# Performance work log

Hardware: AMD Instinct MI355X
Metric: run time of the kernel (lower is better)

Reference implementation:

```python
import jax, jax.numpy as jnp
import numpy as np

T, B, OBS, A, P, NB, H = 32, 256, 1024, 16, 600, 601, 128


def setup_inputs() -> dict:
    key = jax.random.key(0)
    ks = jax.random.split(key, 32)
    f32 = jnp.float32

    def rn(k, shape, scale):
        return jax.random.normal(k, shape, dtype=f32) * scale

    hh = 1.0 / np.sqrt(H)
    inp = {
        "obs_seq": rn(ks[0], (T, B, OBS), 1.0),
        # backbone MLP (512, 512)
        "bb_w1": rn(ks[1], (OBS, 512), 1.0 / np.sqrt(OBS)), "bb_b1": jnp.zeros((512,), f32),
        "bb_w2": rn(ks[2], (512, 512), 1.0 / np.sqrt(512)), "bb_b2": jnp.zeros((512,), f32),
        # feedforward heads (final layers init std=0.01, bias 0 per module)
        "pol_w": rn(ks[3], (512, A), 0.01), "pol_b": jnp.zeros((A,), f32),
        "y_w": rn(ks[4], (512, P), 0.01), "y_b": jnp.zeros((P,), f32),
        "ci_w": rn(ks[5], (512, H), 1.0 / np.sqrt(512)), "ci_b": jnp.zeros((H,), f32),
        # LSTMCell(A, 128): gate order i,f,g,o as in torch
        "w_ih": rn(ks[6], (A, 4 * H), hh), "w_hh": rn(ks[7], (H, 4 * H), hh),
        "b_ih": rn(ks[8], (4 * H,), hh), "b_hh": rn(ks[9], (4 * H,), hh),
        # z / q / aux_pi MLPs: Linear(128,128) -> ReLU -> Linear(128, out)
        "z_w1": rn(ks[10], (H, H), hh), "z_b1": jnp.zeros((H,), f32),
        "z_w2": rn(ks[11], (H, P), 0.01), "z_b2": jnp.zeros((P,), f32),
        "q_w1": rn(ks[12], (H, H), hh), "q_b1": jnp.zeros((H,), f32),
        "q_w2": rn(ks[13], (H, NB), 0.01), "q_b2": jnp.zeros((NB,), f32),
        "a_w1": rn(ks[14], (H, H), hh), "a_b1": jnp.zeros((H,), f32),
        "a_w2": rn(ks[15], (H, A), 0.01), "a_b2": jnp.zeros((A,), f32),
    }
    return inp


def reference(obs_seq, bb_w1, bb_b1, bb_w2, bb_b2, pol_w, pol_b, y_w, y_b,
              ci_w, ci_b, w_ih, w_hh, b_ih, b_hh,
              z_w1, z_b1, z_w2, z_b2, q_w1, q_b1, q_w2, q_b2,
              a_w1, a_b1, a_w2, a_b2):
    Tn, Bn = obs_seq.shape[:2]
    x = obs_seq.reshape(Tn * Bn, -1)  # feedforward across time: fold T into batch
    emb = jax.nn.relu(jax.nn.relu(x @ bb_w1 + bb_b1) @ bb_w2 + bb_b2)  # [N,512]
    logits = emb @ pol_w + pol_b  # [N,A]
    y = emb @ y_w + y_b           # [N,P]
    c0 = emb @ ci_w + ci_b        # [N,H]
    h0 = jnp.tanh(c0)

    # one_hot(a) @ W_ih^T == row a of W_ih (input-to-gate contribution per action)
    in_gates = w_ih + b_ih  # [A, 4H]

    def step(carry, ig):
        h, c = carry
        g = ig + h @ w_hh + b_hh  # [N,4H]
        i, f, gg, o = jnp.split(g, 4, axis=-1)  # torch gate order i,f,g,o
        c = jax.nn.sigmoid(f) * c + jax.nn.sigmoid(i) * jnp.tanh(gg)
        h = jax.nn.sigmoid(o) * jnp.tanh(c)
        return (h, c), h

    _, h_all = jax.lax.scan(step, (h0, c0), in_gates)  # [A, N, H]

    def mlp(hx, w1, b1, w2, b2):
        return jax.nn.relu(hx @ w1 + b1) @ w2 + b2

    def to_tba(arr):
        Aa, N, D = arr.shape
        return arr.reshape(Aa, Tn, Bn, D).transpose(1, 2, 0, 3)  # [T,B,A,D]

    z = to_tba(mlp(h_all, z_w1, z_b1, z_w2, z_b2))
    q = to_tba(mlp(h_all, q_w1, q_b1, q_w2, q_b2))
    aux_pi = to_tba(mlp(h_all, a_w1, a_b1, a_w2, a_b2))
    return (logits.reshape(Tn, Bn, -1), y.reshape(Tn, Bn, -1), z, q, aux_pi)
```

## Files before the change

kernel.cpp:

```cpp
#include <hip/hip_runtime.h>
#include <stdint.h>

typedef short bf16x8 __attribute__((ext_vector_type(8)));
typedef float f32x4 __attribute__((ext_vector_type(4)));
typedef unsigned short u16x4 __attribute__((ext_vector_type(4)));

__device__ __forceinline__ unsigned short f2b(float f) {
  union { float f; unsigned u; } v; v.f = f;
  unsigned r = v.u + 0x7fffu + ((v.u >> 16) & 1u);
  return (unsigned short)(r >> 16);
}
__device__ __forceinline__ float fsigm(float x) { return 1.f / (1.f + __expf(-x)); }
__device__ __forceinline__ float ftanh(float x) {
  float t = __expf(-2.f * fabsf(x));
  float r = (1.f - t) / (1.f + t);
  return copysignf(r, x);
}

struct TD { const float* in; unsigned short* out; int R, C; };
struct TDs { TD d[12]; };

__global__ __launch_bounds__(256) void tconv_all(TDs ds) {
  TD t = ds.d[blockIdx.z];
  int c0 = blockIdx.x * 32, r0 = blockIdx.y * 32;
  if (c0 >= t.C || r0 >= t.R) return;
  __shared__ float tl[32][33];
  int tx = threadIdx.x & 31, ty = threadIdx.x >> 5;
  #pragma unroll
  for (int i = 0; i < 32; i += 8) {
    int r = r0 + ty + i, c = c0 + tx;
    tl[ty + i][tx] = (r < t.R && c < t.C) ? t.in[(size_t)r * t.C + c] : 0.f;
  }
  __syncthreads();
  #pragma unroll
  for (int i = 0; i < 32; i += 8) {
    int c = c0 + ty + i, r = r0 + tx;
    if (c < t.C && r < t.R) t.out[(size_t)c * t.R + r] = f2b(tl[tx][ty + i]);
  }
}

__global__ __launch_bounds__(256) void conv_k(const float* __restrict__ in,
                                              unsigned short* __restrict__ out, int n) {
  int i = (blockIdx.x * 256 + threadIdx.x) * 8;
  if (i >= n) return;
  float4 a = *(const float4*)(in + i);
  float4 b = *(const float4*)(in + i + 4);
  bf16x8 v;
  v[0] = (short)f2b(a.x); v[1] = (short)f2b(a.y); v[2] = (short)f2b(a.z); v[3] = (short)f2b(a.w);
  v[4] = (short)f2b(b.x); v[5] = (short)f2b(b.y); v[6] = (short)f2b(b.z); v[7] = (short)f2b(b.w);
  *(bf16x8*)(out + i) = v;
}

template <int ACT, bool OBF16>
__global__ __launch_bounds__(256) void gemm_k(const unsigned short* __restrict__ A,
                                              const unsigned short* __restrict__ BT,
                                              const float* __restrict__ bias,
                                              void* __restrict__ Cp,
                                              int M, int N, int K, int ldC) {
  __shared__ unsigned short As[64][40];
  __shared__ unsigned short Bs[64][40];
  const int tid = threadIdx.x;
  const int n0 = blockIdx.x * 64;
  const int m0 = blockIdx.y * 64;
  const int wid = tid >> 6, lane = tid & 63;
  const int wm = (wid >> 1) * 32, wn = (wid & 1) * 32;
  const int lr = lane & 15, lk = lane >> 4;
  const int sr = tid >> 2, sc = (tid & 3) * 8;

  f32x4 acc[2][2] = {};

  for (int k0 = 0; k0 < K; k0 += 32) {
    *(bf16x8*)&As[sr][sc] = *(const bf16x8*)(A + (size_t)(m0 + sr) * K + k0 + sc);
    {
      int n = n0 + sr;
      bf16x8 v = {};
      if (n < N) v = *(const bf16x8*)(BT + (size_t)n * K + k0 + sc);
      *(bf16x8*)&Bs[sr][sc] = v;
    }
    __syncthreads();
    bf16x8 af[2], bfr[2];
    #pragma unroll
    for (int mi = 0; mi < 2; mi++) af[mi] = *(const bf16x8*)&As[wm + mi * 16 + lr][lk * 8];
    #pragma unroll
    for (int ni = 0; ni < 2; ni++) bfr[ni] = *(const bf16x8*)&Bs[wn + ni * 16 + lr][lk * 8];
    #pragma unroll
    for (int mi = 0; mi < 2; mi++)
      #pragma unroll
      for (int ni = 0; ni < 2; ni++)
        acc[mi][ni] = __builtin_amdgcn_mfma_f32_16x16x32_bf16(af[mi], bfr[ni], acc[mi][ni], 0, 0, 0);
    __syncthreads();
  }

  #pragma unroll
  for (int mi = 0; mi < 2; mi++)
    #pragma unroll
    for (int ni = 0; ni < 2; ni++) {
      int col = n0 + wn + ni * 16 + lr;
      if (col >= N) continue;
      float bv = bias[col];
      #pragma unroll
      for (int r = 0; r < 4; r++) {
        int row = m0 + wm + mi * 16 + lk * 4 + r;
        float v = acc[mi][ni][r] + bv;
        if (ACT == 1) v = fmaxf(v, 0.f);
        if (OBF16) ((unsigned short*)Cp)[(size_t)row * ldC + col] = f2b(v);
        else       ((float*)Cp)[(size_t)row * ldC + col] = v;
      }
    }
}

__global__ __launch_bounds__(1024) void lstm_k(const float* __restrict__ c0,
                                               const unsigned short* __restrict__ whhT,
                                               const float* __restrict__ w_ih,
                                               const float* __restrict__ b_ih,
                                               const float* __restrict__ b_hh,
                                               unsigned short* __restrict__ h_all) {
  __shared__ float G[32][516];
  __shared__ float cst[32][128];
  __shared__ unsigned short hst[32][136];
  const int tid = threadIdx.x, lane = tid & 63, wid = tid >> 6;
  const int r0 = blockIdx.x * 32;
  const int lr = lane & 15, lk = lane >> 4;

  bf16x8 wv[2][4];
  #pragma unroll
  for (int nj = 0; nj < 2; nj++)
    #pragma unroll
    for (int ks = 0; ks < 4; ks++)
      wv[nj][ks] = *(const bf16x8*)(whhT + (size_t)(wid * 32 + nj * 16 + lr) * 128 + ks * 32 + lk * 8);

  const int j = tid & 127;
  const int rb = tid >> 7;
  const float bs0 = b_ih[j]       + b_hh[j];
  const float bs1 = b_ih[j + 128] + b_hh[j + 128];
  const float bs2 = b_ih[j + 256] + b_hh[j + 256];
  const float bs3 = b_ih[j + 384] + b_hh[j + 384];

  {
    int r = tid >> 5, j4 = (tid & 31) * 4;
    float4 c4 = *(const float4*)(c0 + (size_t)(r0 + r) * 128 + j4);
    *(f32x4*)&cst[r][j4] = f32x4{c4.x, c4.y, c4.z, c4.w};
    u16x4 h4;
    h4[0] = f2b(ftanh(c4.x)); h4[1] = f2b(ftanh(c4.y));
    h4[2] = f2b(ftanh(c4.z)); h4[3] = f2b(ftanh(c4.w));
    *(u16x4*)&hst[r][j4] = h4;
  }
  __syncthreads();

  for (int a = 0; a < 16; a++) {
    f32x4 acc[2][2] = {};
    #pragma unroll
    for (int ks = 0; ks < 4; ks++) {
      bf16x8 af0 = *(const bf16x8*)&hst[lr][ks * 32 + lk * 8];
      bf16x8 af1 = *(const bf16x8*)&hst[16 + lr][ks * 32 + lk * 8];
      #pragma unroll
      for (int nj = 0; nj < 2; nj++) {
        acc[0][nj] = __builtin_amdgcn_mfma_f32_16x16x32_bf16(af0, wv[nj][ks], acc[0][nj], 0, 0, 0);
        acc[1][nj] = __builtin_amdgcn_mfma_f32_16x16x32_bf16(af1, wv[nj][ks], acc[1][nj], 0, 0, 0);
      }
    }
    #pragma unroll
    for (int mi = 0; mi < 2; mi++)
      #pragma unroll
      for (int nj = 0; nj < 2; nj++)
        #pragma unroll
        for (int rr = 0; rr < 4; rr++)
          G[mi * 16 + lk * 4 + rr][wid * 32 + nj * 16 + lr] = acc[mi][nj][rr];
    __syncthreads();

    const float* ig = w_ih + a * 512;
    const float ig0 = ig[j], ig1 = ig[j + 128], ig2 = ig[j + 256], ig3 = ig[j + 384];
    #pragma unroll
    for (int it = 0; it < 4; it++) {
      int r = rb + it * 8;
      float gi = G[r][j]       + ig0 + bs0;
      float gf = G[r][j + 128] + ig1 + bs1;
      float gg = G[r][j + 256] + ig2 + bs2;
      float go = G[r][j + 384] + ig3 + bs3;
      float c = cst[r][j];
      float cn = fsigm(gf) * c + fsigm(gi) * ftanh(gg);
      float h = fsigm(go) * ftanh(cn);
      cst[r][j] = cn;
      unsigned short hb = f2b(h);
      hst[r][j] = hb;
      h_all[((size_t)(r0 + r) * 16 + a) * 128 + j] = hb;
    }
    __syncthreads();
  }
}

__global__ __launch_bounds__(256, 4) void heads_k(
    const unsigned short* __restrict__ hall,
    const unsigned short* __restrict__ w1cat,
    const unsigned short* __restrict__ w2cat,
    const float* __restrict__ zb1, const float* __restrict__ qb1, const float* __restrict__ ab1,
    const float* __restrict__ zb2, const float* __restrict__ qb2, const float* __restrict__ ab2,
    float* __restrict__ oz, float* __restrict__ oq, float* __restrict__ oa) {
  __shared__ unsigned short hs[64][136];
  __shared__ unsigned short hd[64][136];
  const int tid = threadIdx.x;
  const int bid = blockIdx.x;
  const int nb = (bid & 7) * 256 + (bid >> 3);
  const int r0 = nb * 64;
  const int lane = tid & 63, wid = tid >> 6;
  const int lr = lane & 15, lk = lane >> 4;

  {
    int row = tid >> 2, cb = (tid & 3) * 8;
    #pragma unroll
    for (int it = 0; it < 4; it++) {
      int col = cb + it * 32;
      *(bf16x8*)&hs[row][col] = *(const bf16x8*)(hall + (size_t)(r0 + row) * 128 + col);
    }
  }
  __syncthreads();

  const float* B1a[3] = {zb1, qb1, ab1};
  const float* B2a[3] = {zb2, qb2, ab2};
  float*       OOa[3] = {oz, oq, oa};

  #pragma unroll
  for (int hi = 0; hi < 3; hi++) {
    const int NF = (hi == 0) ? 38 : (hi == 1) ? 38 : 1;
    const int Nh = (hi == 0) ? 600 : (hi == 1) ? 601 : 16;
    const int so = (hi == 0) ? 0 : (hi == 1) ? 600 : 1201;
    const float* b1 = B1a[hi];
    const float* b2 = B2a[hi];
    float* Oh = OOa[hi];

    {
      bf16x8 w1v[2][4];
      #pragma unroll
      for (int j = 0; j < 2; j++) {
        int col = (wid * 2 + j) * 16 + lr;
        #pragma unroll
        for (int ks = 0; ks < 4; ks++)
          w1v[j][ks] = *(const bf16x8*)(w1cat + (size_t)(hi * 128 + col) * 128 + ks * 32 + lk * 8);
      }
      f32x4 hacc[2][4] = {};
      #pragma unroll
      for (int ks = 0; ks < 4; ks++) {
        bf16x8 av[4];
        #pragma unroll
        for (int mi = 0; mi < 4; mi++)
          av[mi] = *(const bf16x8*)&hs[mi * 16 + lr][ks * 32 + lk * 8];
        #pragma unroll
        for (int j = 0; j < 2; j++)
          #pragma unroll
          for (int mi = 0; mi < 4; mi++)
            hacc[j][mi] = __builtin_amdgcn_mfma_f32_16x16x32_bf16(av[mi], w1v[j][ks], hacc[j][mi], 0, 0, 0);
      }
      #pragma unroll
      for (int j = 0; j < 2; j++) {
        int col = (wid * 2 + j) * 16 + lr;
        float bb = b1[col];
        #pragma unroll
        for (int mi = 0; mi < 4; mi++)
          #pragma unroll
          for (int rr = 0; rr < 4; rr++)
            hd[mi * 16 + lk * 4 + rr][col] = f2b(fmaxf(hacc[j][mi][rr] + bb, 0.f));
      }
    }
    __syncthreads();

    {
      bf16x8 hda[4][4];
      #pragma unroll
      for (int mi = 0; mi < 4; mi++)
        #pragma unroll
        for (int ks = 0; ks < 4; ks++)
          hda[mi][ks] = *(const bf16x8*)&hd[mi * 16 + lr][ks * 32 + lk * 8];

      bf16x8 bvA[4], bvB[4];
      int f = wid;
      if (f < NF) {
        int bc = min(f * 16 + lr, Nh - 1);
        #pragma unroll
        for (int ks = 0; ks < 4; ks++)
          bvA[ks] = *(const bf16x8*)(w2cat + (size_t)(so + bc) * 128 + ks * 32 + lk * 8);
      }
      for (; f < NF; f += 4) {
        int fn = f + 4;
        if (fn < NF) {
          int bc = min(fn * 16 + lr, Nh - 1);
          #pragma unroll
          for (int ks = 0; ks < 4; ks++)
            bvB[ks] = *(const bf16x8*)(w2cat + (size_t)(so + bc) * 128 + ks * 32 + lk * 8);
        }
        f32x4 oacc[4] = {};
        #pragma unroll
        for (int ks = 0; ks < 4; ks++)
          #pragma unroll
          for (int mi = 0; mi < 4; mi++)
            oacc[mi] = __builtin_amdgcn_mfma_f32_16x16x32_bf16(hda[mi][ks], bvA[ks], oacc[mi], 0, 0, 0);
        int col = f * 16 + lr;
        if (col < Nh) {
          float bb = b2[col];
          #pragma unroll
          for (int mi = 0; mi < 4; mi++)
            #pragma unroll
            for (int rr = 0; rr < 4; rr++)
              Oh[(size_t)(r0 + mi * 16 + lk * 4 + rr) * Nh + col] = oacc[mi][rr] + bb;
        }
        #pragma unroll
        for (int ks = 0; ks < 4; ks++) bvA[ks] = bvB[ks];
      }
    }
    __syncthreads();
  }
}

extern "C" void kernel_launch(void* const* d_in, const int* in_sizes, int n_in,
                              void* d_out, int out_size, void* d_ws, size_t ws_size,
                              hipStream_t stream) {
  const float* obs   = (const float*)d_in[0];
  const float* bb_w1 = (const float*)d_in[1];
  const float* bb_b1 = (const float*)d_in[2];
  const float* bb_w2 = (const float*)d_in[3];
  const float* bb_b2 = (const float*)d_in[4];
  const float* pol_w = (const float*)d_in[5];
  const float* pol_b = (const float*)d_in[6];
  const float* y_w   = (const float*)d_in[7];
  const float* y_b   = (const float*)d_in[8];
  const float* ci_w  = (const float*)d_in[9];
  const float* ci_b  = (const float*)d_in[10];
  const float* w_ih  = (const float*)d_in[11];
  const float* w_hh  = (const float*)d_in[12];
  const float* b_ih  = (const float*)d_in[13];
  const float* b_hh  = (const float*)d_in[14];
  const float* z_w1  = (const float*)d_in[15];
  const float* z_b1  = (const float*)d_in[16];
  const float* z_w2  = (const float*)d_in[17];
  const float* z_b2  = (const float*)d_in[18];
  const float* q_w1  = (const float*)d_in[19];
  const float* q_b1  = (const float*)d_in[20];
  const float* q_w2  = (const float*)d_in[21];
  const float* q_b2  = (const float*)d_in[22];
  const float* a_w1  = (const float*)d_in[23];
  const float* a_b1  = (const float*)d_in[24];
  const float* a_w2  = (const float*)d_in[25];
  const float* a_b2  = (const float*)d_in[26];

  float* out = (float*)d_out;
  float* out_logits = out;
  float* out_y      = out + 131072;
  float* out_z      = out + 5046272;
  float* out_q      = out + 83689472;
  float* out_a      = out + 162463744;

  uint8_t* ws = (uint8_t*)d_ws;
  size_t off = 0;
  auto alc = [&](size_t bytes) -> void* {
    void* p = ws + off;
    off = (off + bytes + 255) & ~(size_t)255;
    return p;
  };
  unsigned short* W1T  = (unsigned short*)alc((size_t)512 * 1024 * 2);
  unsigned short* W2T  = (unsigned short*)alc((size_t)512 * 512 * 2);
  unsigned short* polT = (unsigned short*)alc((size_t)16 * 512 * 2);
  unsigned short* yT   = (unsigned short*)alc((size_t)600 * 512 * 2);
  unsigned short* ciT  = (unsigned short*)alc((size_t)128 * 512 * 2);
  unsigned short* whhT = (unsigned short*)alc((size_t)512 * 128 * 2);
  unsigned short* zw1T = (unsigned short*)alc((size_t)128 * 128 * 2);
  unsigned short* qw1T = (unsigned short*)alc((size_t)128 * 128 * 2);
  unsigned short* aw1T = (unsigned short*)alc((size_t)128 * 128 * 2);
  unsigned short* zw2T = (unsigned short*)alc((size_t)600 * 128 * 2);
  unsigned short* qw2T = (unsigned short*)alc((size_t)601 * 128 * 2);
  unsigned short* aw2T = (unsigned short*)alc((size_t)16 * 128 * 2);
  unsigned short* obsb = (unsigned short*)alc((size_t)8192 * 1024 * 2);
  unsigned short* hid1 = (unsigned short*)alc((size_t)8192 * 512 * 2);
  unsigned short* emb  = (unsigned short*)alc((size_t)8192 * 512 * 2);
  float*          c0b  = (float*)alc((size_t)8192 * 128 * 4);
  unsigned short* hall = (unsigned short*)alc((size_t)8192 * 16 * 128 * 2);
  (void)ws_size; (void)in_sizes; (void)n_in; (void)out_size;

  dim3 B256(256);

  TDs td;
  td.d[0]  = {bb_w1, W1T, 1024, 512};
  td.d[1]  = {bb_w2, W2T, 512, 512};
  td.d[2]  = {pol_w, polT, 512, 16};
  td.d[3]  = {y_w,   yT,   512, 600};
  td.d[4]  = {ci_w,  ciT,  512, 128};
  td.d[5]  = {w_hh,  whhT, 128, 512};
  td.d[6]  = {z_w1,  zw1T, 128, 128};
  td.d[7]  = {z_w2,  zw2T, 128, 600};
  td.d[8]  = {q_w1,  qw1T, 128, 128};
  td.d[9]  = {q_w2,  qw2T, 128, 601};
  td.d[10] = {a_w1,  aw1T, 128, 128};
  td.d[11] = {a_w2,  aw2T, 128, 16};
  tconv_all<<<dim3(19, 32, 12), B256, 0, stream>>>(td);

  conv_k<<<dim3(4096), B256, 0, stream>>>(obs, obsb, 8192 * 1024);

  gemm_k<1, true><<<dim3(8, 128), B256, 0, stream>>>(obsb, W1T, bb_b1, hid1, 8192, 512, 1024, 512);
  gemm_k<1, true><<<dim3(8, 128), B256, 0, stream>>>(hid1, W2T, bb_b2, emb,  8192, 512, 512,  512);
  gemm_k<0, false><<<dim3(1, 128),  B256, 0, stream>>>(emb, polT, pol_b, out_logits, 8192, 16,  512, 16);
  gemm_k<0, false><<<dim3(10, 128), B256, 0, stream>>>(emb, yT,   y_b,   out_y,      8192, 600, 512, 600);
  gemm_k<0, false><<<dim3(2, 128),  B256, 0, stream>>>(emb, ciT,  ci_b,  c0b,        8192, 128, 512, 128);
  lstm_k<<<dim3(256), dim3(1024), 0, stream>>>(c0b, whhT, w_ih, b_ih, b_hh, hall);
  heads_k<<<dim3(2048), B256, 0, stream>>>(hall,
                                           zw1T, zw2T,
                                           z_b1, q_b1, a_b1,
                                           z_b2, q_b2, a_b2,
                                           out_z, out_q, out_a);
}
```

Baseline: 493.9 us.

## Fuse backbone, heads, LSTM and output MLPs into one persistent megakernel

Replaces the obs conversion, five GEMM launches, the LSTM kernel and the heads kernel with a single kernel. Each 1024-thread block owns 32 rows and keeps obs, hidden, embedding, LSTM state and head activations in shared memory, so the large bf16 intermediates (obs, hid1, emb, c0, h_all) are never written to or read from global memory. The head MLPs run inside the LSTM loop for each action step, and large outputs use nontemporal stores. The cost is that only 256 blocks cover the whole problem, leaving low parallelism per CU for the large backbone GEMMs, and weights are re-read from global or L2 by every block.

```diff
diff --git a/kernel.cpp b/kernel.cpp
--- a/kernel.cpp
+++ b/kernel.cpp
@@ -15,6 +15,9 @@
   float t = __expf(-2.f * fabsf(x));
   float r = (1.f - t) / (1.f + t);
   return copysignf(r, x);
+}
+__device__ __forceinline__ void nts4(float* p, f32x4 v) {
+  __builtin_nontemporal_store(v, (f32x4*)p);
 }
 
 struct TD { const float* in; unsigned short* out; int R, C; };
@@ -39,95 +42,170 @@
   }
 }
 
-__global__ __launch_bounds__(256) void conv_k(const float* __restrict__ in,
-                                              unsigned short* __restrict__ out, int n) {
-  int i = (blockIdx.x * 256 + threadIdx.x) * 8;
-  if (i >= n) return;
-  float4 a = *(const float4*)(in + i);
-  float4 b = *(const float4*)(in + i + 4);
-  bf16x8 v;
-  v[0] = (short)f2b(a.x); v[1] = (short)f2b(a.y); v[2] = (short)f2b(a.z); v[3] = (short)f2b(a.w);
-  v[4] = (short)f2b(b.x); v[5] = (short)f2b(b.y); v[6] = (short)f2b(b.z); v[7] = (short)f2b(b.w);
-  *(bf16x8*)(out + i) = v;
-}
-
-template <int ACT, bool OBF16>
-__global__ __launch_bounds__(256) void gemm_k(const unsigned short* __restrict__ A,
-                                              const unsigned short* __restrict__ BT,
-                                              const float* __restrict__ bias,
-                                              void* __restrict__ Cp,
-                                              int M, int N, int K, int ldC) {
-  __shared__ unsigned short As[64][40];
-  __shared__ unsigned short Bs[64][40];
+__global__ __launch_bounds__(1024, 4) void mega_k(
+    const float* __restrict__ obs,
+    const unsigned short* __restrict__ W1T, const float* __restrict__ bb1,
+    const unsigned short* __restrict__ W2T, const float* __restrict__ bb2,
+    const unsigned short* __restrict__ polT, const float* __restrict__ pol_b,
+    const unsigned short* __restrict__ yT,  const float* __restrict__ y_b,
+    const unsigned short* __restrict__ ciT, const float* __restrict__ ci_b,
+    const unsigned short* __restrict__ whhT,
+    const float* __restrict__ w_ih, const float* __restrict__ b_ih, const float* __restrict__ b_hh,
+    const unsigned short* __restrict__ w1cat,
+    const float* __restrict__ zb1, const float* __restrict__ qb1, const float* __restrict__ ab1,
+    const unsigned short* __restrict__ w2cat,
+    const float* __restrict__ zb2, const float* __restrict__ qb2, const float* __restrict__ ab2,
+    float* __restrict__ oL, float* __restrict__ oY,
+    float* __restrict__ oz, float* __restrict__ oq, float* __restrict__ oa) {
+  __shared__ __align__(16) uint8_t smem[125440];
+  unsigned short (*obsS)[520] = (unsigned short(*)[520])(smem);
+  unsigned short (*h1S)[520]  = (unsigned short(*)[520])(smem + 33280);
+  unsigned short (*embS)[520] = (unsigned short(*)[520])(smem + 66560);
+  unsigned short (*hstS)[136] = (unsigned short(*)[136])(smem + 99840);
+  float          (*cstS)[132] = (float(*)[132])(smem + 108544);
+  float          (*GS)[516]   = (float(*)[516])(smem);
+  unsigned short (*hdS)[392]  = (unsigned short(*)[392])(smem + 66560);
+
   const int tid = threadIdx.x;
-  const int n0 = blockIdx.x * 64;
-  const int m0 = blockIdx.y * 64;
-  const int wid = tid >> 6, lane = tid & 63;
-  const int wm = (wid >> 1) * 32, wn = (wid & 1) * 32;
+  const int w = tid >> 6, lane = tid & 63;
   const int lr = lane & 15, lk = lane >> 4;
-  const int sr = tid >> 2, sc = (tid & 3) * 8;
-
-  f32x4 acc[2][2] = {};
-
-  for (int k0 = 0; k0 < K; k0 += 32) {
-    *(bf16x8*)&As[sr][sc] = *(const bf16x8*)(A + (size_t)(m0 + sr) * K + k0 + sc);
-    {
-      int n = n0 + sr;
-      bf16x8 v = {};
-      if (n < N) v = *(const bf16x8*)(BT + (size_t)n * K + k0 + sc);
-      *(bf16x8*)&Bs[sr][sc] = v;
-    }
-    __syncthreads();
-    bf16x8 af[2], bfr[2];
-    #pragma unroll
-    for (int mi = 0; mi < 2; mi++) af[mi] = *(const bf16x8*)&As[wm + mi * 16 + lr][lk * 8];
-    #pragma unroll
-    for (int ni = 0; ni < 2; ni++) bfr[ni] = *(const bf16x8*)&Bs[wn + ni * 16 + lr][lk * 8];
-    #pragma unroll
-    for (int mi = 0; mi < 2; mi++)
-      #pragma unroll
-      for (int ni = 0; ni < 2; ni++)
-        acc[mi][ni] = __builtin_amdgcn_mfma_f32_16x16x32_bf16(af[mi], bfr[ni], acc[mi][ni], 0, 0, 0);
-    __syncthreads();
-  }
-
+  const int r0 = blockIdx.x * 32;
+
+  {
+    f32x4 acc[2][2] = {};
+    #pragma unroll
+    for (int p = 0; p < 2; p++) {
+      {
+        int row = tid >> 5, cbase = (tid & 31) * 4;
+        const float* src = obs + (size_t)(r0 + row) * 1024 + p * 512;
+        #pragma unroll
+        for (int i = 0; i < 4; i++) {
+          int c = cbase + i * 128;
+          float4 f = *(const float4*)(src + c);
+          u16x4 v; v[0] = f2b(f.x); v[1] = f2b(f.y); v[2] = f2b(f.z); v[3] = f2b(f.w);
+          *(u16x4*)&obsS[row][c] = v;
+        }
+      }
+      __syncthreads();
+      for (int ks = 0; ks < 16; ks++) {
+        bf16x8 av[2], bv[2];
+        #pragma unroll
+        for (int cf = 0; cf < 2; cf++)
+          av[cf] = *(const bf16x8*)(W1T + (size_t)(32 * w + 16 * cf + lr) * 1024 + p * 512 + ks * 32 + lk * 8);
+        #pragma unroll
+        for (int rf = 0; rf < 2; rf++)
+          bv[rf] = *(const bf16x8*)&obsS[16 * rf + lr][ks * 32 + lk * 8];
+        #pragma unroll
+        for (int cf = 0; cf < 2; cf++)
+          #pragma unroll
+          for (int rf = 0; rf < 2; rf++)
+            acc[rf][cf] = __builtin_amdgcn_mfma_f32_16x16x32_bf16(av[cf], bv[rf], acc[rf][cf], 0, 0, 0);
+      }
+      __syncthreads();
+    }
+    #pragma unroll
+    for (int rf = 0; rf < 2; rf++)
+      #pragma unroll
+      for (int cf = 0; cf < 2; cf++) {
+        int col = 32 * w + 16 * cf + lk * 4;
+        f32x4 bb = *(const f32x4*)(bb1 + col);
+        u16x4 v;
+        #pragma unroll
+        for (int rr = 0; rr < 4; rr++) v[rr] = f2b(fmaxf(acc[rf][cf][rr] + bb[rr], 0.f));
+        *(u16x4*)&h1S[16 * rf + lr][col] = v;
+      }
+  }
+  __syncthreads();
+
+  {
+    f32x4 acc[2][2] = {};
+    for (int ks = 0; ks < 16; ks++) {
+      bf16x8 av[2], bv[2];
+      #pragma unroll
+      for (int cf = 0; cf < 2; cf++)
+        av[cf] = *(const bf16x8*)(W2T + (size_t)(32 * w + 16 * cf + lr) * 512 + ks * 32 + lk * 8);
+      #pragma unroll
+      for (int rf = 0; rf < 2; rf++)
+        bv[rf] = *(const bf16x8*)&h1S[16 * rf + lr][ks * 32 + lk * 8];
+      #pragma unroll
+      for (int cf = 0; cf < 2; cf++)
+        #pragma unroll
+        for (int rf = 0; rf < 2; rf++)
+          acc[rf][cf] = __builtin_amdgcn_mfma_f32_16x16x32_bf16(av[cf], bv[rf], acc[rf][cf], 0, 0, 0);
+    }
+    #pragma unroll
+    for (int rf = 0; rf < 2; rf++)
+      #pragma unroll
+      for (int cf = 0; cf < 2; cf++) {
+        int col = 32 * w + 16 * cf + lk * 4;
+        f32x4 bb = *(const f32x4*)(bb2 + col);
+        u16x4 v;
+        #pragma unroll
+        for (int rr = 0; rr < 4; rr++) v[rr] = f2b(fmaxf(acc[rf][cf][rr] + bb[rr], 0.f));
+        *(u16x4*)&embS[16 * rf + lr][col] = v;
+      }
+  }
+  __syncthreads();
+
+  if (w < 8) {
+    f32x4 acc[2] = {};
+    for (int ks = 0; ks < 16; ks++) {
+      bf16x8 av = *(const bf16x8*)(ciT + (size_t)(16 * w + lr) * 512 + ks * 32 + lk * 8);
+      #pragma unroll
+      for (int rf = 0; rf < 2; rf++) {
+        bf16x8 bv = *(const bf16x8*)&embS[16 * rf + lr][ks * 32 + lk * 8];
+        acc[rf] = __builtin_amdgcn_mfma_f32_16x16x32_bf16(av, bv, acc[rf], 0, 0, 0);
+      }
+    }
+    int col = 16 * w + lk * 4;
+    f32x4 bb = *(const f32x4*)(ci_b + col);
+    #pragma unroll
+    for (int rf = 0; rf < 2; rf++) {
+      f32x4 c = acc[rf] + bb;
+      *(f32x4*)&cstS[16 * rf + lr][col] = c;
+      u16x4 h; 
+      #pragma unroll
+      for (int rr = 0; rr < 4; rr++) h[rr] = f2b(ftanh(c[rr]));
+      *(u16x4*)&hstS[16 * rf + lr][col] = h;
+    }
+  } else if (w == 8) {
+    f32x4 acc[2] = {};
+    for (int ks = 0; ks < 16; ks++) {
+      bf16x8 av = *(const bf16x8*)(polT + (size_t)lr * 512 + ks * 32 + lk * 8);
+      #pragma unroll
+      for (int rf = 0; rf < 2; rf++) {
+        bf16x8 bv = *(const bf16x8*)&embS[16 * rf + lr][ks * 32 + lk * 8];
+        acc[rf] = __builtin_amdgcn_mfma_f32_16x16x32_bf16(av, bv, acc[rf], 0, 0, 0);
+      }
+    }
+    f32x4 bb = *(const f32x4*)(pol_b + lk * 4);
+    #pragma unroll
+    for (int rf = 0; rf < 2; rf++)
+      *(f32x4*)(oL + (size_t)(r0 + 16 * rf + lr) * 16 + lk * 4) = acc[rf] + bb;
+  }
   #pragma unroll
-  for (int mi = 0; mi < 2; mi++)
-    #pragma unroll
-    for (int ni = 0; ni < 2; ni++) {
-      int col = n0 + wn + ni * 16 + lr;
-      if (col >= N) continue;
-      float bv = bias[col];
-      #pragma unroll
-      for (int r = 0; r < 4; r++) {
-        int row = m0 + wm + mi * 16 + lk * 4 + r;
-        float v = acc[mi][ni][r] + bv;
-        if (ACT == 1) v = fmaxf(v, 0.f);
-        if (OBF16) ((unsigned short*)Cp)[(size_t)row * ldC + col] = f2b(v);
-        else       ((float*)Cp)[(size_t)row * ldC + col] = v;
-      }
-    }
-}
-
-__global__ __launch_bounds__(1024) void lstm_k(const float* __restrict__ c0,
-                                               const unsigned short* __restrict__ whhT,
-                                               const float* __restrict__ w_ih,
-                                               const float* __restrict__ b_ih,
-                                               const float* __restrict__ b_hh,
-                                               unsigned short* __restrict__ h_all) {
-  __shared__ float G[32][516];
-  __shared__ float cst[32][128];
-  __shared__ unsigned short hst[32][136];
-  const int tid = threadIdx.x, lane = tid & 63, wid = tid >> 6;
-  const int r0 = blockIdx.x * 32;
-  const int lr = lane & 15, lk = lane >> 4;
-
-  bf16x8 wv[2][4];
-  #pragma unroll
-  for (int nj = 0; nj < 2; nj++)
-    #pragma unroll
-    for (int ks = 0; ks < 4; ks++)
-      wv[nj][ks] = *(const bf16x8*)(whhT + (size_t)(wid * 32 + nj * 16 + lr) * 128 + ks * 32 + lk * 8);
+  for (int ii = 0; ii < 3; ii++) {
+    int f = w + ii * 16;
+    if (f >= 38) break;
+    int yrow = min(f * 16 + lr, 599);
+    f32x4 acc[2] = {};
+    for (int ks = 0; ks < 16; ks++) {
+      bf16x8 av = *(const bf16x8*)(yT + (size_t)yrow * 512 + ks * 32 + lk * 8);
+      #pragma unroll
+      for (int rf = 0; rf < 2; rf++) {
+        bf16x8 bv = *(const bf16x8*)&embS[16 * rf + lr][ks * 32 + lk * 8];
+        acc[rf] = __builtin_amdgcn_mfma_f32_16x16x32_bf16(av, bv, acc[rf], 0, 0, 0);
+      }
+    }
+    int col = f * 16 + lk * 4;
+    if (col + 3 < 600) {
+      f32x4 bb = *(const f32x4*)(y_b + col);
+      #pragma unroll
+      for (int rf = 0; rf < 2; rf++)
+        nts4(oY + (size_t)(r0 + 16 * rf + lr) * 600 + col, acc[rf] + bb);
+    }
+  }
+  __syncthreads();
 
   const int j = tid & 127;
   const int rb = tid >> 7;
@@ -136,174 +214,125 @@
   const float bs2 = b_ih[j + 256] + b_hh[j + 256];
   const float bs3 = b_ih[j + 384] + b_hh[j + 384];
 
-  {
-    int r = tid >> 5, j4 = (tid & 31) * 4;
-    float4 c4 = *(const float4*)(c0 + (size_t)(r0 + r) * 128 + j4);
-    *(f32x4*)&cst[r][j4] = f32x4{c4.x, c4.y, c4.z, c4.w};
-    u16x4 h4;
-    h4[0] = f2b(ftanh(c4.x)); h4[1] = f2b(ftanh(c4.y));
-    h4[2] = f2b(ftanh(c4.z)); h4[3] = f2b(ftanh(c4.w));
-    *(u16x4*)&hst[r][j4] = h4;
-  }
-  __syncthreads();
-
   for (int a = 0; a < 16; a++) {
-    f32x4 acc[2][2] = {};
-    #pragma unroll
-    for (int ks = 0; ks < 4; ks++) {
-      bf16x8 af0 = *(const bf16x8*)&hst[lr][ks * 32 + lk * 8];
-      bf16x8 af1 = *(const bf16x8*)&hst[16 + lr][ks * 32 + lk * 8];
-      #pragma unroll
-      for (int nj = 0; nj < 2; nj++) {
-        acc[0][nj] = __builtin_amdgcn_mfma_f32_16x16x32_bf16(af0, wv[nj][ks], acc[0][nj], 0, 0, 0);
-        acc[1][nj] = __builtin_amdgcn_mfma_f32_16x16x32_bf16(af1, wv[nj][ks], acc[1][nj], 0, 0, 0);
-      }
-    }
-    #pragma unroll
-    for (int mi = 0; mi < 2; mi++)
-      #pragma unroll
-      for (int nj = 0; nj < 2; nj++)
-        #pragma unroll
-        for (int rr = 0; rr < 4; rr++)
-          G[mi * 16 + lk * 4 + rr][wid * 32 + nj * 16 + lr] = acc[mi][nj][rr];
-    __syncthreads();
-
-    const float* ig = w_ih + a * 512;
-    const float ig0 = ig[j], ig1 = ig[j + 128], ig2 = ig[j + 256], ig3 = ig[j + 384];
-    #pragma unroll
-    for (int it = 0; it < 4; it++) {
-      int r = rb + it * 8;
-      float gi = G[r][j]       + ig0 + bs0;
-      float gf = G[r][j + 128] + ig1 + bs1;
-      float gg = G[r][j + 256] + ig2 + bs2;
-      float go = G[r][j + 384] + ig3 + bs3;
-      float c = cst[r][j];
-      float cn = fsigm(gf) * c + fsigm(gi) * ftanh(gg);
-      float h = fsigm(go) * ftanh(cn);
-      cst[r][j] = cn;
-      unsigned short hb = f2b(h);
-      hst[r][j] = hb;
-      h_all[((size_t)(r0 + r) * 16 + a) * 128 + j] = hb;
-    }
-    __syncthreads();
-  }
-}
-
-__global__ __launch_bounds__(256, 4) void heads_k(
-    const unsigned short* __restrict__ hall,
-    const unsigned short* __restrict__ w1cat,
-    const unsigned short* __restrict__ w2cat,
-    const float* __restrict__ zb1, const float* __restrict__ qb1, const float* __restrict__ ab1,
-    const float* __restrict__ zb2, const float* __restrict__ qb2, const float* __restrict__ ab2,
-    float* __restrict__ oz, float* __restrict__ oq, float* __restrict__ oa) {
-  __shared__ unsigned short hs[64][136];
-  __shared__ unsigned short hd[64][136];
-  const int tid = threadIdx.x;
-  const int bid = blockIdx.x;
-  const int nb = (bid & 7) * 256 + (bid >> 3);
-  const int r0 = nb * 64;
-  const int lane = tid & 63, wid = tid >> 6;
-  const int lr = lane & 15, lk = lane >> 4;
-
-  {
-    int row = tid >> 2, cb = (tid & 3) * 8;
-    #pragma unroll
-    for (int it = 0; it < 4; it++) {
-      int col = cb + it * 32;
-      *(bf16x8*)&hs[row][col] = *(const bf16x8*)(hall + (size_t)(r0 + row) * 128 + col);
-    }
-  }
-  __syncthreads();
-
-  const float* B1a[3] = {zb1, qb1, ab1};
-  const float* B2a[3] = {zb2, qb2, ab2};
-  float*       OOa[3] = {oz, oq, oa};
-
-  #pragma unroll
-  for (int hi = 0; hi < 3; hi++) {
-    const int NF = (hi == 0) ? 38 : (hi == 1) ? 38 : 1;
-    const int Nh = (hi == 0) ? 600 : (hi == 1) ? 601 : 16;
-    const int so = (hi == 0) ? 0 : (hi == 1) ? 600 : 1201;
-    const float* b1 = B1a[hi];
-    const float* b2 = B2a[hi];
-    float* Oh = OOa[hi];
-
     {
-      bf16x8 w1v[2][4];
-      #pragma unroll
-      for (int j = 0; j < 2; j++) {
-        int col = (wid * 2 + j) * 16 + lr;
-        #pragma unroll
-        for (int ks = 0; ks < 4; ks++)
-          w1v[j][ks] = *(const bf16x8*)(w1cat + (size_t)(hi * 128 + col) * 128 + ks * 32 + lk * 8);
-      }
-      f32x4 hacc[2][4] = {};
+      f32x4 acc[2][2] = {};
       #pragma unroll
       for (int ks = 0; ks < 4; ks++) {
-        bf16x8 av[4];
-        #pragma unroll
-        for (int mi = 0; mi < 4; mi++)
-          av[mi] = *(const bf16x8*)&hs[mi * 16 + lr][ks * 32 + lk * 8];
-        #pragma unroll
-        for (int j = 0; j < 2; j++)
-          #pragma unroll
-          for (int mi = 0; mi < 4; mi++)
-            hacc[j][mi] = __builtin_amdgcn_mfma_f32_16x16x32_bf16(av[mi], w1v[j][ks], hacc[j][mi], 0, 0, 0);
-      }
-      #pragma unroll
-      for (int j = 0; j < 2; j++) {
-        int col = (wid * 2 + j) * 16 + lr;
-        float bb = b1[col];
-        #pragma unroll
-        for (int mi = 0; mi < 4; mi++)
+        bf16x8 af0 = *(const bf16x8*)&hstS[lr][ks * 32 + lk * 8];
+        bf16x8 af1 = *(const bf16x8*)&hstS[16 + lr][ks * 32 + lk * 8];
+        #pragma unroll
+        for (int nj = 0; nj < 2; nj++) {
+          bf16x8 wv = *(const bf16x8*)(whhT + (size_t)(32 * w + 16 * nj + lr) * 128 + ks * 32 + lk * 8);
+          acc[0][nj] = __builtin_amdgcn_mfma_f32_16x16x32_bf16(af0, wv, acc[0][nj], 0, 0, 0);
+          acc[1][nj] = __builtin_amdgcn_mfma_f32_16x16x32_bf16(af1, wv, acc[1][nj], 0, 0, 0);
+        }
+      }
+      #pragma unroll
+      for (int rf = 0; rf < 2; rf++)
+        #pragma unroll
+        for (int nj = 0; nj < 2; nj++)
           #pragma unroll
           for (int rr = 0; rr < 4; rr++)
-            hd[mi * 16 + lk * 4 + rr][col] = f2b(fmaxf(hacc[j][mi][rr] + bb, 0.f));
-      }
+            GS[rf * 16 + lk * 4 + rr][32 * w + 16 * nj + lr] = acc[rf][nj][rr];
     }
     __syncthreads();
 
     {
-      bf16x8 hda[4][4];
-      #pragma unroll
-      for (int mi = 0; mi < 4; mi++)
+      const float* ig = w_ih + a * 512;
+      const float ig0 = ig[j], ig1 = ig[j + 128], ig2 = ig[j + 256], ig3 = ig[j + 384];
+      #pragma unroll
+      for (int it = 0; it < 4; it++) {
+        int r = rb + it * 8;
+        float gi = GS[r][j]       + ig0 + bs0;
+        float gf = GS[r][j + 128] + ig1 + bs1;
+        float gg = GS[r][j + 256] + ig2 + bs2;
+        float go = GS[r][j + 384] + ig3 + bs3;
+        float c = cstS[r][j];
+        float cn = fsigm(gf) * c + fsigm(gi) * ftanh(gg);
+        float h = fsigm(go) * ftanh(cn);
+        cstS[r][j] = cn;
+        hstS[r][j] = f2b(h);
+      }
+    }
+    __syncthreads();
+
+    {
+      bf16x8 hb[2][4];
+      #pragma unroll
+      for (int rf = 0; rf < 2; rf++)
         #pragma unroll
         for (int ks = 0; ks < 4; ks++)
-          hda[mi][ks] = *(const bf16x8*)&hd[mi * 16 + lr][ks * 32 + lk * 8];
-
-      bf16x8 bvA[4], bvB[4];
-      int f = wid;
-      if (f < NF) {
-        int bc = min(f * 16 + lr, Nh - 1);
+          hb[rf][ks] = *(const bf16x8*)&hstS[16 * rf + lr][ks * 32 + lk * 8];
+      #pragma unroll
+      for (int ii = 0; ii < 2; ii++) {
+        int f = w + ii * 16;
+        if (f >= 24) break;
+        int head = f >> 3;
+        const float* b1 = (head == 0) ? zb1 : (head == 1) ? qb1 : ab1;
+        bf16x8 w1v[4];
         #pragma unroll
         for (int ks = 0; ks < 4; ks++)
-          bvA[ks] = *(const bf16x8*)(w2cat + (size_t)(so + bc) * 128 + ks * 32 + lk * 8);
-      }
-      for (; f < NF; f += 4) {
-        int fn = f + 4;
-        if (fn < NF) {
-          int bc = min(fn * 16 + lr, Nh - 1);
-          #pragma unroll
-          for (int ks = 0; ks < 4; ks++)
-            bvB[ks] = *(const bf16x8*)(w2cat + (size_t)(so + bc) * 128 + ks * 32 + lk * 8);
-        }
-        f32x4 oacc[4] = {};
+          w1v[ks] = *(const bf16x8*)(w1cat + (size_t)(f * 16 + lr) * 128 + ks * 32 + lk * 8);
+        f32x4 acc[2] = {};
         #pragma unroll
         for (int ks = 0; ks < 4; ks++)
           #pragma unroll
-          for (int mi = 0; mi < 4; mi++)
-            oacc[mi] = __builtin_amdgcn_mfma_f32_16x16x32_bf16(hda[mi][ks], bvA[ks], oacc[mi], 0, 0, 0);
-        int col = f * 16 + lr;
-        if (col < Nh) {
-          float bb = b2[col];
+          for (int rf = 0; rf < 2; rf++)
+            acc[rf] = __builtin_amdgcn_mfma_f32_16x16x32_bf16(w1v[ks], hb[rf][ks], acc[rf], 0, 0, 0);
+        int col = (f & 7) * 16 + lk * 4;
+        f32x4 bb = *(const f32x4*)(b1 + col);
+        #pragma unroll
+        for (int rf = 0; rf < 2; rf++) {
+          u16x4 v;
           #pragma unroll
-          for (int mi = 0; mi < 4; mi++)
-            #pragma unroll
-            for (int rr = 0; rr < 4; rr++)
-              Oh[(size_t)(r0 + mi * 16 + lk * 4 + rr) * Nh + col] = oacc[mi][rr] + bb;
-        }
-        #pragma unroll
-        for (int ks = 0; ks < 4; ks++) bvA[ks] = bvB[ks];
+          for (int rr = 0; rr < 4; rr++) v[rr] = f2b(fmaxf(acc[rf][rr] + bb[rr], 0.f));
+          *(u16x4*)&hdS[16 * rf + lr][f * 16 + lk * 4] = v;
+        }
+      }
+    }
+    __syncthreads();
+
+    #pragma unroll
+    for (int ii = 0; ii < 5; ii++) {
+      int f = w + ii * 16;
+      if (f > 76) break;
+      int head = (f < 38) ? 0 : (f < 76) ? 1 : 2;
+      int fz = f - ((head == 0) ? 0 : (head == 1) ? 38 : 76);
+      int Nh = (head == 0) ? 600 : (head == 1) ? 601 : 16;
+      int wbase = (head == 0) ? 0 : (head == 1) ? 600 : 1201;
+      const float* b2 = (head == 0) ? zb2 : (head == 1) ? qb2 : ab2;
+      float* O = (head == 0) ? oz : (head == 1) ? oq : oa;
+
+      int wrow = wbase + min(fz * 16 + lr, Nh - 1);
+      f32x4 acc[2] = {};
+      #pragma unroll
+      for (int ks = 0; ks < 4; ks++) {
+        bf16x8 w2v = *(const bf16x8*)(w2cat + (size_t)wrow * 128 + ks * 32 + lk * 8);
+        #pragma unroll
+        for (int rf = 0; rf < 2; rf++) {
+          bf16x8 hv = *(const bf16x8*)&hdS[16 * rf + lr][head * 128 + ks * 32 + lk * 8];
+          acc[rf] = __builtin_amdgcn_mfma_f32_16x16x32_bf16(w2v, hv, acc[rf], 0, 0, 0);
+        }
+      }
+      int col = fz * 16 + lk * 4;
+      if (col + 3 < Nh) {
+        f32x4 bb = *(const f32x4*)(b2 + col);
+        #pragma unroll
+        for (int rf = 0; rf < 2; rf++) {
+          size_t orow = (size_t)((r0 + 16 * rf + lr) * 16 + a);
+          f32x4 v = acc[rf] + bb;
+          if (head == 1) __builtin_memcpy(O + orow * Nh + col, &v, 16);
+          else           nts4(O + orow * Nh + col, v);
+        }
+      } else if (col < Nh) {
+        #pragma unroll
+        for (int rf = 0; rf < 2; rf++) {
+          size_t orow = (size_t)((r0 + 16 * rf + lr) * 16 + a);
+          #pragma unroll
+          for (int rr = 0; rr < 4; rr++)
+            if (col + rr < Nh) O[orow * Nh + col + rr] = acc[rf][rr] + b2[col + rr];
+        }
       }
     }
     __syncthreads();
@@ -367,12 +396,8 @@
   unsigned short* zw2T = (unsigned short*)alc((size_t)600 * 128 * 2);
   unsigned short* qw2T = (unsigned short*)alc((size_t)601 * 128 * 2);
   unsigned short* aw2T = (unsigned short*)alc((size_t)16 * 128 * 2);
-  unsigned short* obsb = (unsigned short*)alc((size_t)8192 * 1024 * 2);
-  unsigned short* hid1 = (unsigned short*)alc((size_t)8192 * 512 * 2);
-  unsigned short* emb  = (unsigned short*)alc((size_t)8192 * 512 * 2);
-  float*          c0b  = (float*)alc((size_t)8192 * 128 * 4);
-  unsigned short* hall = (unsigned short*)alc((size_t)8192 * 16 * 128 * 2);
   (void)ws_size; (void)in_sizes; (void)n_in; (void)out_size;
+  (void)zw1T; (void)qw1T; (void)aw1T; (void)qw2T; (void)aw2T;
 
   dim3 B256(256);
 
@@ -391,17 +416,11 @@
   td.d[11] = {a_w2,  aw2T, 128, 16};
   tconv_all<<<dim3(19, 32, 12), B256, 0, stream>>>(td);
 
-  conv_k<<<dim3(4096), B256, 0, stream>>>(obs, obsb, 8192 * 1024);
-
-  gemm_k<1, true><<<dim3(8, 128), B256, 0, stream>>>(obsb, W1T, bb_b1, hid1, 8192, 512, 1024, 512);
-  gemm_k<1, true><<<dim3(8, 128), B256, 0, stream>>>(hid1, W2T, bb_b2, emb,  8192, 512, 512,  512);
-  gemm_k<0, false><<<dim3(1, 128),  B256, 0, stream>>>(emb, polT, pol_b, out_logits, 8192, 16,  512, 16);
-  gemm_k<0, false><<<dim3(10, 128), B256, 0, stream>>>(emb, yT,   y_b,   out_y,      8192, 600, 512, 600);
-  gemm_k<0, false><<<dim3(2, 128),  B256, 0, stream>>>(emb, ciT,  ci_b,  c0b,        8192, 128, 512, 128);
-  lstm_k<<<dim3(256), dim3(1024), 0, stream>>>(c0b, whhT, w_ih, b_ih, b_hh, hall);
-  heads_k<<<dim3(2048), B256, 0, stream>>>(hall,
-                                           zw1T, zw2T,
-                                           z_b1, q_b1, a_b1,
-                                           z_b2, q_b2, a_b2,
-                                           out_z, out_q, out_a);
-}
+  mega_k<<<dim3(256), dim3(1024), 0, stream>>>(
+      obs, W1T, bb_b1, W2T, bb_b2,
+      polT, pol_b, yT, y_b, ciT, ci_b,
+      whhT, w_ih, b_ih, b_hh,
+      zw1T, z_b1, q_b1, a_b1,
+      zw2T, z_b2, q_b2, a_b2,
+      out_logits, out_y, out_z, out_q, out_a);
+}
```

New measurement: 579.4 us. 17.3% more time.
